# Kernel optimization log

Hardware: AMD Instinct MI355X
Metric: run time of the kernel (lower is better)

The kernel has to match this reference:

```python
import jax, jax.numpy as jnp
import numpy as np

NUM_GRAPHS = 64

def _glorot(key, shape):
    fan_in, fan_out = shape
    lim = (6.0 / (fan_in + fan_out)) ** 0.5
    return jax.random.uniform(key, shape, jnp.float32, -lim, lim)

def setup_inputs() -> dict:
    key = jax.random.key(0)
    ks = jax.random.split(key, 16)
    N, F = 100000, 200000
    pos = jax.random.normal(ks[0], (N, 3), jnp.float32)
    batch = jnp.sort(jax.random.randint(ks[1], (N,), 0, NUM_GRAPHS))
    face = jax.random.randint(ks[2], (3, F), 0, N)
    # PointNetLayer MLPs: Linear(in+3, out) -> ReLU -> Linear(out, out)
    W1a = _glorot(ks[3], (6, 32));  b1a = jnp.zeros((32,), jnp.float32)
    W1b = _glorot(ks[4], (32, 32)); b1b = jnp.zeros((32,), jnp.float32)
    W2a = _glorot(ks[5], (35, 32)); b2a = jnp.zeros((32,), jnp.float32)
    W2b = _glorot(ks[6], (32, 32)); b2b = jnp.zeros((32,), jnp.float32)
    W3a = _glorot(ks[7], (35, 64)); b3a = jnp.zeros((64,), jnp.float32)
    W3b = _glorot(ks[8], (64, 64)); b3b = jnp.zeros((64,), jnp.float32)
    Wc  = _glorot(ks[9], (64, 41)); bc  = jnp.zeros((41,), jnp.float32)
    return dict(pos=pos, batch=batch, face=face,
                W1a=W1a, b1a=b1a, W1b=W1b, b1b=b1b,
                W2a=W2a, b2a=b2a, W2b=W2b, b2b=b2b,
                W3a=W3a, b3a=b3a, W3b=W3b, b3b=b3b,
                Wc=Wc, bc=bc)

def _layer(h, pos, src, dst, Wa, ba, Wb, bb, num_nodes):
    # message: mlp(cat([h_j, pos_j - pos_i])), aggregate max into target i
    x = jnp.concatenate([h[src], pos[src] - pos[dst]], axis=-1)  # [E, in+3]
    m = jax.nn.relu(x @ Wa + ba) @ Wb + bb                       # [E, out]
    out = jax.ops.segment_max(m, dst, num_segments=num_nodes)
    return jnp.where(jnp.isneginf(out), 0.0, out)  # PyG max-aggr fills empties with 0

def reference(pos, batch, face, W1a, b1a, W1b, b1b, W2a, b2a, W2b, b2b,
              W3a, b3a, W3b, b3b, Wc, bc):
    N = pos.shape[0]
    f0, f1, f2 = face[0], face[1], face[2]
    src = jnp.concatenate([f0, f0, f1, f1, f2, f2])  # edge_index[0] (j)
    dst = jnp.concatenate([f1, f2, f2, f0, f0, f1])  # edge_index[1] (i)
    # per-point L1 normalization (F.normalize p=1, dim=0, eps=1e-12)
    pos = pos / jnp.maximum(jnp.sum(jnp.abs(pos), axis=1, keepdims=True), 1e-12)
    h = jax.nn.relu(_layer(pos, pos, src, dst, W1a, b1a, W1b, b1b, N))
    h = jax.nn.relu(_layer(h, pos, src, dst, W2a, b2a, W2b, b2b, N))
    h = jax.nn.relu(_layer(h, pos, src, dst, W3a, b3a, W3b, b3b, N))
    g = jax.ops.segment_max(h, batch, num_segments=NUM_GRAPHS)  # global_max_pool
    g = jnp.where(jnp.isneginf(g), 0.0, g)
    return g @ Wc + bc  # [NUM_GRAPHS, 41]
```

## Files before the change

### kernel.cpp

```cpp
#include <hip/hip_runtime.h>


__global__ __launch_bounds__(256) void prep_kernel(
    const float* __restrict__ pos, float* __restrict__ posn, int N,
    const float* __restrict__ W1a, const float* __restrict__ W2a,
    const float* __restrict__ W3a,
    float* __restrict__ W1aT, float* __restrict__ W2aT, float* __restrict__ W3aT)
{
    int idx = blockIdx.x * blockDim.x + threadIdx.x;
    if (idx < N) {
        float x = pos[idx * 3 + 0];
        float y = pos[idx * 3 + 1];
        float z = pos[idx * 3 + 2];
        float s = fmaxf(fabsf(x) + fabsf(y) + fabsf(z), 1e-12f);
        float inv = 1.0f / s;
        posn[idx * 3 + 0] = x * inv;
        posn[idx * 3 + 1] = y * inv;
        posn[idx * 3 + 2] = z * inv;
    }
    if (blockIdx.x == 0) {
        for (int t = threadIdx.x; t < 6 * 32; t += blockDim.x) {
            int i = t / 32, k = t % 32;
            W1aT[k * 6 + i] = W1a[t];
        }
        for (int t = threadIdx.x; t < 35 * 32; t += blockDim.x) {
            int i = t / 32, k = t % 32;
            W2aT[k * 35 + i] = W2a[t];
        }
        for (int t = threadIdx.x; t < 35 * 64; t += blockDim.x) {
            int i = t / 64, k = t % 64;
            W3aT[k * 35 + i] = W3a[t];
        }
    }
}

__global__ __launch_bounds__(256) void count_kernel(
    const int* __restrict__ face, int F3, int* __restrict__ deg)
{
    int t = blockIdx.x * blockDim.x + threadIdx.x;
    if (t < F3) atomicAdd(&deg[face[t]], 2);
}

__global__ __launch_bounds__(256) void hist_kernel(
    const int* __restrict__ deg, int N, int* __restrict__ hist)
{
    __shared__ int lh[256];
    lh[threadIdx.x] = 0;
    __syncthreads();
    int stride = gridDim.x * blockDim.x;
    for (int t = blockIdx.x * blockDim.x + threadIdx.x; t < N; t += stride)
        atomicAdd(&lh[min(deg[t], 255)], 1);
    __syncthreads();
    int c = lh[threadIdx.x];
    if (c) atomicAdd(&hist[threadIdx.x], c);
}

__global__ __launch_bounds__(256) void binscan_kernel(
    const int* __restrict__ hist, int* __restrict__ cursor)
{
    __shared__ int sh[256];
    int t = threadIdx.x;
    int rt = 255 - t;
    int v = hist[rt];
    sh[t] = v;
    __syncthreads();
    for (int off = 1; off < 256; off <<= 1) {
        int tv = (t >= off) ? sh[t - off] : 0;
        __syncthreads();
        sh[t] += tv;
        __syncthreads();
    }
    cursor[rt] = sh[t] - v;
}

__global__ __launch_bounds__(256) void scatter_kernel(
    const int* __restrict__ deg, int N, int* __restrict__ cursor,
    int* __restrict__ perm)
{
    __shared__ int lh[256];
    __shared__ int lbase[256];
    int tid = threadIdx.x;
    lh[tid] = 0;
    __syncthreads();
    int t = blockIdx.x * blockDim.x + tid;
    int b = 0, r = 0;
    bool valid = (t < N);
    if (valid) {
        b = min(deg[t], 255);
        r = atomicAdd(&lh[b], 1);
    }
    __syncthreads();
    int c = lh[tid];
    if (c) lbase[tid] = atomicAdd(&cursor[tid], c);
    __syncthreads();
    if (valid) perm[lbase[b] + r] = t;
}

__global__ __launch_bounds__(256) void scan_reduce(
    const int* __restrict__ deg, int N, int* __restrict__ partial)
{
    __shared__ int sh[256];
    int b0 = blockIdx.x * 1024;
    int sum = 0;
    #pragma unroll
    for (int j = 0; j < 4; j++) {
        int idx = b0 + j * 256 + threadIdx.x;
        if (idx < N) sum += deg[idx];
    }
    sh[threadIdx.x] = sum;
    __syncthreads();
    for (int off = 128; off > 0; off >>= 1) {
        if (threadIdx.x < off) sh[threadIdx.x] += sh[threadIdx.x + off];
        __syncthreads();
    }
    if (threadIdx.x == 0) partial[blockIdx.x] = sh[0];
}

__global__ __launch_bounds__(1024) void scan_partials(
    int* __restrict__ partial, int B, int* __restrict__ totalp)
{
    __shared__ int sh[1024];
    int t = threadIdx.x;
    int v = (t < B) ? partial[t] : 0;
    sh[t] = v;
    __syncthreads();
    for (int off = 1; off < 1024; off <<= 1) {
        int tv = (t >= off) ? sh[t - off] : 0;
        __syncthreads();
        sh[t] += tv;
        __syncthreads();
    }
    if (t < B) partial[t] = sh[t] - v;
    if (t == 1023) *totalp = sh[1023];
}

__global__ __launch_bounds__(256) void scan_apply(
    const int* __restrict__ deg, int N, const int* __restrict__ partial,
    int* __restrict__ indptr, int* __restrict__ ecur)
{
    __shared__ int sh[256];
    int t = threadIdx.x;
    int i0 = blockIdx.x * 1024 + t * 4;
    int d[4];
    int s = 0;
    #pragma unroll
    for (int j = 0; j < 4; j++) {
        d[j] = (i0 + j < N) ? deg[i0 + j] : 0;
        s += d[j];
    }
    sh[t] = s;
    __syncthreads();
    for (int off = 1; off < 256; off <<= 1) {
        int tv = (t >= off) ? sh[t - off] : 0;
        __syncthreads();
        sh[t] += tv;
        __syncthreads();
    }
    int run = partial[blockIdx.x] + sh[t] - s;
    #pragma unroll
    for (int j = 0; j < 4; j++) {
        int idx = i0 + j;
        if (idx < N) {
            indptr[idx] = run;
            ecur[idx] = run;
        }
        run += d[j];
    }
}

__global__ __launch_bounds__(256) void fill_kernel(
    const int* __restrict__ face, int F, int* __restrict__ cursor,
    int* __restrict__ srcids)
{
    int t = blockIdx.x * blockDim.x + threadIdx.x;
    if (t >= 3 * F) return;
    int r = t / F;
    int f = t - r * F;
    int v = face[t];
    int r1 = r + 1; if (r1 == 3) r1 = 0;
    int r2 = r + 2; if (r2 >= 3) r2 -= 3;
    int a = face[r1 * F + f];
    int b = face[r2 * F + f];
    int base = atomicAdd(&cursor[v], 2);
    srcids[base] = a;
    srcids[base + 1] = b;
}

template <int INH, int OUT>
__global__ __launch_bounds__(256) void uv_kernel(
    const float* __restrict__ h, const float* __restrict__ posn,
    const float* __restrict__ WaT, const float* __restrict__ ba,
    float* __restrict__ u, float* __restrict__ v, int N)
{
    constexpr int IN = INH + 3;
    int n = blockIdx.x * blockDim.x + threadIdx.x;
    if (n >= N) return;
    float x[IN];
    if constexpr (INH % 4 == 0) {
        const float4* hp = (const float4*)(h + (size_t)n * INH);
        #pragma unroll
        for (int i4 = 0; i4 < INH / 4; i4++) {
            float4 t = hp[i4];
            x[i4 * 4 + 0] = t.x;
            x[i4 * 4 + 1] = t.y;
            x[i4 * 4 + 2] = t.z;
            x[i4 * 4 + 3] = t.w;
        }
    } else {
        #pragma unroll
        for (int i = 0; i < INH; i++) x[i] = h[(size_t)n * INH + i];
    }
    x[INH + 0] = posn[n * 3 + 0];
    x[INH + 1] = posn[n * 3 + 1];
    x[INH + 2] = posn[n * 3 + 2];

    float4* up = (float4*)(u + (size_t)n * OUT);
    float4* vp = (float4*)(v + (size_t)n * OUT);
    #pragma unroll 2
    for (int k4 = 0; k4 < OUT / 4; k4++) {
        float uu[4], vv[4];
        #pragma unroll
        for (int j = 0; j < 4; j++) {
            int k = k4 * 4 + j;
            float uk = ba[k];
            #pragma unroll
            for (int i = 0; i < IN; i++)
                uk = fmaf(x[i], WaT[k * IN + i], uk);
            uu[j] = uk;
            float vk = x[INH] * WaT[k * IN + INH];
            vk = fmaf(x[INH + 1], WaT[k * IN + INH + 1], vk);
            vk = fmaf(x[INH + 2], WaT[k * IN + INH + 2], vk);
            vv[j] = vk;
        }
        float4 u4; u4.x = uu[0]; u4.y = uu[1]; u4.z = uu[2]; u4.w = uu[3];
        float4 v4; v4.x = vv[0]; v4.y = vv[1]; v4.z = vv[2]; v4.w = vv[3];
        up[k4] = u4;
        vp[k4] = v4;
    }
}

template <int OUT, int MINW>
__global__ __launch_bounds__(256, MINW) void gather_kernel(
    const float* __restrict__ u, const float* __restrict__ v,
    const int* __restrict__ perm, const int* __restrict__ indptr,
    const int* __restrict__ srcids, const float* __restrict__ Wb,
    const float* __restrict__ bb, float* __restrict__ hout, int N)
{
    int gt = blockIdx.x * blockDim.x + threadIdx.x;
    int gslot = gt >> 2;
    int t = gt & 3;
    if (gslot >= N) return;
    int n = perm[gslot];
    const float4* vp = (const float4*)(v + (size_t)n * OUT);
    int e0 = indptr[n], e1 = indptr[n + 1];

    float M[OUT];
    #pragma unroll
    for (int o = 0; o < OUT; o++) M[o] = -1e30f;

    for (int e = e0 + t; e < e1; e += 4) {
        int src = srcids[e];
        const float4* up = (const float4*)(u + (size_t)src * OUT);
        float acc[OUT];
        #pragma unroll
        for (int o = 0; o < OUT; o++) acc[o] = 0.0f;
        #pragma unroll 2
        for (int k4 = 0; k4 < OUT / 4; k4++) {
            float4 u4 = up[k4];
            float4 v4 = vp[k4];
            float hk;
            hk = fmaxf(u4.x - v4.x, 0.0f);
            #pragma unroll
            for (int o = 0; o < OUT; o++)
                acc[o] = fmaf(hk, Wb[(k4 * 4 + 0) * OUT + o], acc[o]);
            hk = fmaxf(u4.y - v4.y, 0.0f);
            #pragma unroll
            for (int o = 0; o < OUT; o++)
                acc[o] = fmaf(hk, Wb[(k4 * 4 + 1) * OUT + o], acc[o]);
            hk = fmaxf(u4.z - v4.z, 0.0f);
            #pragma unroll
            for (int o = 0; o < OUT; o++)
                acc[o] = fmaf(hk, Wb[(k4 * 4 + 2) * OUT + o], acc[o]);
            hk = fmaxf(u4.w - v4.w, 0.0f);
            #pragma unroll
            for (int o = 0; o < OUT; o++)
                acc[o] = fmaf(hk, Wb[(k4 * 4 + 3) * OUT + o], acc[o]);
        }
        #pragma unroll
        for (int o = 0; o < OUT; o++) M[o] = fmaxf(M[o], acc[o]);
    }

    #pragma unroll
    for (int m = 1; m < 4; m <<= 1) {
        #pragma unroll
        for (int o = 0; o < OUT; o++)
            M[o] = fmaxf(M[o], __shfl_xor(M[o], m));
    }

    constexpr int CH = OUT / 4;
    #pragma unroll
    for (int tt = 0; tt < 4; tt++) {
        if (t == tt) {
            float* outp = hout + (size_t)n * OUT + tt * CH;
            #pragma unroll
            for (int o4 = 0; o4 < CH / 4; o4++) {
                float4 w;
                w.x = fmaxf(M[tt * CH + o4 * 4 + 0] + bb[tt * CH + o4 * 4 + 0], 0.0f);
                w.y = fmaxf(M[tt * CH + o4 * 4 + 1] + bb[tt * CH + o4 * 4 + 1], 0.0f);
                w.z = fmaxf(M[tt * CH + o4 * 4 + 2] + bb[tt * CH + o4 * 4 + 2], 0.0f);
                w.w = fmaxf(M[tt * CH + o4 * 4 + 3] + bb[tt * CH + o4 * 4 + 3], 0.0f);
                ((float4*)outp)[o4] = w;
            }
        }
    }
}

__global__ __launch_bounds__(256) void pool_kernel(
    const float* __restrict__ h3, const int* __restrict__ batch, int N,
    float* __restrict__ g)
{
    int o = threadIdx.x & 63;
    int sub = threadIdx.x >> 6;
    int n0 = blockIdx.x * 256;
    int nend = min(n0 + 256, N);
    int cur = -1;
    float run = 0.0f;
    for (int n = n0 + sub; n < nend; n += 4) {
        int b = batch[n];
        if (b != cur) {
            if (cur >= 0) atomicMax((int*)&g[cur * 64 + o], __float_as_int(run));
            cur = b;
            run = 0.0f;
        }
        run = fmaxf(run, h3[(size_t)n * 64 + o]);
    }
    if (cur >= 0) atomicMax((int*)&g[cur * 64 + o], __float_as_int(run));
}

__global__ __launch_bounds__(256) void head_kernel(
    const float* __restrict__ g, const float* __restrict__ Wc,
    const float* __restrict__ bc, float* __restrict__ out)
{
    int idx = blockIdx.x * blockDim.x + threadIdx.x;
    if (idx >= 64 * 41) return;
    int bg = idx / 41;
    int o = idx - bg * 41;
    float acc = bc[o];
    #pragma unroll 8
    for (int k = 0; k < 64; k++)
        acc = fmaf(g[bg * 64 + k], Wc[k * 41 + o], acc);
    out[idx] = acc;
}

extern "C" void kernel_launch(void* const* d_in, const int* in_sizes, int n_in,
                              void* d_out, int out_size, void* d_ws, size_t ws_size,
                              hipStream_t stream)
{
    const float* pos   = (const float*)d_in[0];
    const int*   batch = (const int*)d_in[1];
    const int*   face  = (const int*)d_in[2];
    const float* W1a = (const float*)d_in[3];
    const float* b1a = (const float*)d_in[4];
    const float* W1b = (const float*)d_in[5];
    const float* b1b = (const float*)d_in[6];
    const float* W2a = (const float*)d_in[7];
    const float* b2a = (const float*)d_in[8];
    const float* W2b = (const float*)d_in[9];
    const float* b2b = (const float*)d_in[10];
    const float* W3a = (const float*)d_in[11];
    const float* b3a = (const float*)d_in[12];
    const float* W3b = (const float*)d_in[13];
    const float* b3b = (const float*)d_in[14];
    const float* Wc  = (const float*)d_in[15];
    const float* bc  = (const float*)d_in[16];

    int N = in_sizes[0] / 3;
    int F = in_sizes[2] / 3;

    float* ws   = (float*)d_ws;
    float* posn = ws;
    float* W1aT = posn + (size_t)N * 3;
    float* W2aT = W1aT + 6 * 32;
    float* W3aT = W2aT + 35 * 32;
    float* h3   = W3aT + 35 * 64;
    float* h1   = h3;
    float* h2   = h3 + (size_t)N * 64;
    float* u    = h2 + (size_t)N * 32;
    float* v    = u + (size_t)N * 64;
    float* g    = v + (size_t)N * 64;
    int* deg    = (int*)(g + 64 * 64);
    int* indptr = deg + N;
    int* srcids = indptr + (N + 1);
    int* perm   = srcids + (size_t)6 * F;
    int* hist   = perm + N;
    int* cursor = hist + 256;
    int* ecur   = cursor + 256;
    int* partial = ecur + N;

    hipMemsetAsync(deg, 0, (size_t)N * sizeof(int), stream);
    hipMemsetAsync(hist, 0, 256 * sizeof(int), stream);
    hipMemsetAsync(g, 0, 64 * 64 * sizeof(float), stream);

    prep_kernel<<<(N + 255) / 256, 256, 0, stream>>>(
        pos, posn, N, W1a, W2a, W3a, W1aT, W2aT, W3aT);

    int F3 = 3 * F;
    int gN = (N + 255) / 256;
    int gN4 = ((size_t)N * 4 + 255) / 256;
    int B = (N + 1023) / 1024;
    count_kernel<<<(F3 + 255) / 256, 256, 0, stream>>>(face, F3, deg);
    hist_kernel<<<64, 256, 0, stream>>>(deg, N, hist);
    binscan_kernel<<<1, 256, 0, stream>>>(hist, cursor);
    scatter_kernel<<<gN, 256, 0, stream>>>(deg, N, cursor, perm);
    scan_reduce<<<B, 256, 0, stream>>>(deg, N, partial);
    scan_partials<<<1, 1024, 0, stream>>>(partial, B, indptr + N);
    scan_apply<<<B, 256, 0, stream>>>(deg, N, partial, indptr, ecur);
    fill_kernel<<<(F3 + 255) / 256, 256, 0, stream>>>(face, F, ecur, srcids);

    uv_kernel<3, 32><<<gN, 256, 0, stream>>>(posn, posn, W1aT, b1a, u, v, N);
    gather_kernel<32, 4><<<gN4, 256, 0, stream>>>(
        u, v, perm, indptr, srcids, W1b, b1b, h1, N);
    uv_kernel<32, 32><<<gN, 256, 0, stream>>>(h1, posn, W2aT, b2a, u, v, N);
    gather_kernel<32, 4><<<gN4, 256, 0, stream>>>(
        u, v, perm, indptr, srcids, W2b, b2b, h2, N);
    uv_kernel<32, 64><<<gN, 256, 0, stream>>>(h2, posn, W3aT, b3a, u, v, N);
    gather_kernel<64, 2><<<gN4, 256, 0, stream>>>(
        u, v, perm, indptr, srcids, W3b, b3b, h3, N);

    pool_kernel<<<(N + 255) / 256, 256, 0, stream>>>(h3, batch, N, g);
    head_kernel<<<(64 * 41 + 255) / 256, 256, 0, stream>>>(g, Wc, bc, (float*)d_out);
}
```

Before: 541.5 us.

## Hoist per-node v into registers and remap warps to contiguous degree-sorted chunks

The gather kernel now loads the target node's v vector into registers once (for OUT=32 layers) instead of re-reading it for every edge. It also remaps each 64-lane wavefront to a contiguous chunk of the degree-sorted permutation, with the chunks spread across 64 interleaved groups, to balance work across CUs. The launch-bound occupancy hint for the 32-wide layers drops from 4 to 2 waves to make room for the extra registers. The cost is higher register pressure and lower occupancy.

```diff
diff --git a/kernel.cpp b/kernel.cpp
--- a/kernel.cpp
+++ b/kernel.cpp
@@ -239,21 +239,40 @@
     }
 }
 
-template <int OUT, int MINW>
+template <int OUT, int MINW, bool VH>
 __global__ __launch_bounds__(256, MINW) void gather_kernel(
     const float* __restrict__ u, const float* __restrict__ v,
     const int* __restrict__ perm, const int* __restrict__ indptr,
     const int* __restrict__ srcids, const float* __restrict__ Wb,
     const float* __restrict__ bb, float* __restrict__ hout, int N)
 {
-    int gt = blockIdx.x * blockDim.x + threadIdx.x;
-    int gslot = gt >> 2;
-    int t = gt & 3;
+    int gw = (blockIdx.x * blockDim.x + threadIdx.x) >> 6;
+    int lane = threadIdx.x & 63;
+    int nw = (N + 15) >> 4;
+    int kc = gw & 63, j = gw >> 6;
+    int q = nw >> 6, r = nw & 63;
+    int jmax = (kc < r) ? q : q - 1;
+    if (j > jmax) return;
+    int cbase = (kc < r) ? kc * (q + 1) : r * (q + 1) + (kc - r) * q;
+    int gslot = (cbase + j) * 16 + (lane >> 2);
+    int t = lane & 3;
     if (gslot >= N) return;
     int n = perm[gslot];
     const float4* vp = (const float4*)(v + (size_t)n * OUT);
     int e0 = indptr[n], e1 = indptr[n + 1];
 
+    float vq[VH ? OUT : 1];
+    if constexpr (VH) {
+        #pragma unroll
+        for (int m = 0; m < OUT / 4; m++) {
+            float4 x = vp[m];
+            vq[4 * m + 0] = x.x;
+            vq[4 * m + 1] = x.y;
+            vq[4 * m + 2] = x.z;
+            vq[4 * m + 3] = x.w;
+        }
+    }
+
     float M[OUT];
     #pragma unroll
     for (int o = 0; o < OUT; o++) M[o] = -1e30f;
@@ -267,21 +286,28 @@
         #pragma unroll 2
         for (int k4 = 0; k4 < OUT / 4; k4++) {
             float4 u4 = up[k4];
-            float4 v4 = vp[k4];
+            float vx, vy, vz, vw;
+            if constexpr (VH) {
+                vx = vq[k4 * 4 + 0]; vy = vq[k4 * 4 + 1];
+                vz = vq[k4 * 4 + 2]; vw = vq[k4 * 4 + 3];
+            } else {
+                float4 v4 = vp[k4];
+                vx = v4.x; vy = v4.y; vz = v4.z; vw = v4.w;
+            }
             float hk;
-            hk = fmaxf(u4.x - v4.x, 0.0f);
+            hk = fmaxf(u4.x - vx, 0.0f);
             #pragma unroll
             for (int o = 0; o < OUT; o++)
                 acc[o] = fmaf(hk, Wb[(k4 * 4 + 0) * OUT + o], acc[o]);
-            hk = fmaxf(u4.y - v4.y, 0.0f);
+            hk = fmaxf(u4.y - vy, 0.0f);
             #pragma unroll
             for (int o = 0; o < OUT; o++)
                 acc[o] = fmaf(hk, Wb[(k4 * 4 + 1) * OUT + o], acc[o]);
-            hk = fmaxf(u4.z - v4.z, 0.0f);
+            hk = fmaxf(u4.z - vz, 0.0f);
             #pragma unroll
             for (int o = 0; o < OUT; o++)
                 acc[o] = fmaf(hk, Wb[(k4 * 4 + 2) * OUT + o], acc[o]);
-            hk = fmaxf(u4.w - v4.w, 0.0f);
+            hk = fmaxf(u4.w - vw, 0.0f);
             #pragma unroll
             for (int o = 0; o < OUT; o++)
                 acc[o] = fmaf(hk, Wb[(k4 * 4 + 3) * OUT + o], acc[o]);
@@ -418,13 +444,13 @@
     fill_kernel<<<(F3 + 255) / 256, 256, 0, stream>>>(face, F, ecur, srcids);
 
     uv_kernel<3, 32><<<gN, 256, 0, stream>>>(posn, posn, W1aT, b1a, u, v, N);
-    gather_kernel<32, 4><<<gN4, 256, 0, stream>>>(
+    gather_kernel<32, 2, true><<<gN4, 256, 0, stream>>>(
         u, v, perm, indptr, srcids, W1b, b1b, h1, N);
     uv_kernel<32, 32><<<gN, 256, 0, stream>>>(h1, posn, W2aT, b2a, u, v, N);
-    gather_kernel<32, 4><<<gN4, 256, 0, stream>>>(
+    gather_kernel<32, 2, true><<<gN4, 256, 0, stream>>>(
         u, v, perm, indptr, srcids, W2b, b2b, h2, N);
     uv_kernel<32, 64><<<gN, 256, 0, stream>>>(h2, posn, W3aT, b3a, u, v, N);
-    gather_kernel<64, 2><<<gN4, 256, 0, stream>>>(
+    gather_kernel<64, 2, false><<<gN4, 256, 0, stream>>>(
         u, v, perm, indptr, srcids, W3b, b3b, h3, N);
 
     pool_kernel<<<(N + 255) / 256, 256, 0, stream>>>(h3, batch, N, g);
```

Result: slower. 677.5 us (+25.1%).
